# Kernel tuning notes

Measured on AMD Instinct MI355X. Metric: run time of the kernel, lower is better.

## Reference

```python
import jax, jax.numpy as jnp
import numpy as np

B, T, N, K = 1024, 4096, 2048, 16
M = 1 << K  # per-neuron memory size (use_hashing=False -> 2**k)


def setup_inputs() -> dict:
    key = jax.random.key(0)
    k1, k2, k3 = jax.random.split(key, 3)
    input_bits = jax.random.randint(k1, (B, T), 0, 2, dtype=jnp.int32)          # 0/1 bits
    connections = jax.random.randint(k2, (N, K), 0, T, dtype=jnp.int32)         # fixed wiring
    memory = jax.random.randint(k3, (N, M), 0, 256, dtype=jnp.int32)            # per-neuron RAM contents
    return {"input_bits": input_bits, "connections": connections, "memory": memory}


def reference(input_bits, connections, memory):
    # gather the k wired bits for every neuron: [B, N, K]
    gathered = input_bits[:, connections].astype(jnp.int32)
    # bit weights = powers of two (RAMNeuron._bit_weights), LSB-first
    bit_weights = (jnp.int32(1) << jnp.arange(K, dtype=jnp.int32))              # [K]
    # weighted sum -> memory address per (sample, neuron): [B, N]
    addresses = jnp.sum(gathered * bit_weights, axis=-1)
    # per-neuron memory lookup: memory[n, addresses[b, n]] -> [B, N]
    mems = memory[jnp.arange(N)[None, :], addresses]
    # output is the stored LSB as a bool bit
    return (mems & 1).astype(jnp.bool_)
```

## Files before the change

kernel.cpp:

```cpp
#include <hip/hip_runtime.h>
#include <cstdint>

#define Bc 1024
#define Tc 4096
#define Nc 2048
#define Kc 16
#define Mc 65536
#define ROW_WORDS (Mc / 32)
#define PACKED_WORDS ((size_t)Nc * ROW_WORDS)

__global__ __launch_bounds__(256) void pack_kernel(
    const int* __restrict__ memory, uint32_t* __restrict__ packed)
{
    const size_t w = (size_t)blockIdx.x * 256 + threadIdx.x;
    const int4* src = (const int4*)(memory + w * 32);
    uint32_t bw = 0;
#pragma unroll
    for (int i = 0; i < 8; ++i) {
        const int4 v = src[i];
        bw |= (uint32_t)(v.x & 1) << (i * 4);
        bw |= (uint32_t)(v.y & 1) << (i * 4 + 1);
        bw |= (uint32_t)(v.z & 1) << (i * 4 + 2);
        bw |= (uint32_t)(v.w & 1) << (i * 4 + 3);
    }
    packed[w] = bw;
}

__global__ __launch_bounds__(256) void ram_lookup_packed(
    const int* __restrict__ input_bits,
    const int* __restrict__ connections,
    const uint32_t* __restrict__ packedmem,
    int* __restrict__ out)
{
    __shared__ uint32_t bits[Tc / 32];

    const int b    = blockIdx.x;
    const int tid  = threadIdx.x;
    const int lane = tid & 63;
    const int wave = tid >> 6;

    const int* row = input_bits + (size_t)b * Tc;

#pragma unroll
    for (int i = 0; i < Tc / 256; ++i) {
        const int pos = i * 256 + wave * 64 + lane;
        const unsigned long long m = __ballot(row[pos] & 1);
        if (lane == 0) {
            const int w64 = i * 4 + wave;
            bits[w64 * 2]     = (uint32_t)m;
            bits[w64 * 2 + 1] = (uint32_t)(m >> 32);
        }
    }
    __syncthreads();

    uint32_t addrs[Nc / 256];
#pragma unroll
    for (int i = 0; i < Nc / 256; ++i) {
        const int n = i * 256 + tid;
        const int4* cp = (const int4*)(connections + n * Kc);
        const int4 c0 = cp[0], c1 = cp[1], c2 = cp[2], c3 = cp[3];
        const int c[16] = {c0.x, c0.y, c0.z, c0.w,
                           c1.x, c1.y, c1.z, c1.w,
                           c2.x, c2.y, c2.z, c2.w,
                           c3.x, c3.y, c3.z, c3.w};
        uint32_t a = 0;
#pragma unroll
        for (int k = 0; k < 16; ++k) {
            const uint32_t t = (uint32_t)c[k];
            a |= ((bits[t >> 5] >> (t & 31)) & 1u) << k;
        }
        addrs[i] = a;
    }

    uint32_t words[Nc / 256];
#pragma unroll
    for (int i = 0; i < Nc / 256; ++i) {
        const int n = i * 256 + tid;
        words[i] = packedmem[((size_t)n << 11) + (addrs[i] >> 5)];
    }

#pragma unroll
    for (int i = 0; i < Nc / 256; ++i) {
        out[(size_t)b * Nc + i * 256 + tid] = (int)((words[i] >> (addrs[i] & 31)) & 1u);
    }
}

__global__ __launch_bounds__(256) void ram_lookup_direct(
    const int* __restrict__ input_bits,
    const int* __restrict__ connections,
    const int* __restrict__ memory,
    int* __restrict__ out)
{
    __shared__ uint32_t bits[Tc / 32];
    const int b = blockIdx.x, tid = threadIdx.x;
    const int lane = tid & 63, wave = tid >> 6;
    const int* row = input_bits + (size_t)b * Tc;
#pragma unroll
    for (int i = 0; i < Tc / 256; ++i) {
        const int pos = i * 256 + wave * 64 + lane;
        const unsigned long long m = __ballot(row[pos] & 1);
        if (lane == 0) {
            const int w64 = i * 4 + wave;
            bits[w64 * 2] = (uint32_t)m;
            bits[w64 * 2 + 1] = (uint32_t)(m >> 32);
        }
    }
    __syncthreads();
    uint32_t addrs[Nc / 256];
#pragma unroll
    for (int i = 0; i < Nc / 256; ++i) {
        const int n = i * 256 + tid;
        const int4* cp = (const int4*)(connections + n * Kc);
        const int4 c0 = cp[0], c1 = cp[1], c2 = cp[2], c3 = cp[3];
        const int c[16] = {c0.x, c0.y, c0.z, c0.w, c1.x, c1.y, c1.z, c1.w,
                           c2.x, c2.y, c2.z, c2.w, c3.x, c3.y, c3.z, c3.w};
        uint32_t a = 0;
#pragma unroll
        for (int k = 0; k < 16; ++k) {
            const uint32_t t = (uint32_t)c[k];
            a |= ((bits[t >> 5] >> (t & 31)) & 1u) << k;
        }
        addrs[i] = a;
    }
    int vals[Nc / 256];
#pragma unroll
    for (int i = 0; i < Nc / 256; ++i) {
        const int n = i * 256 + tid;
        vals[i] = memory[(size_t)n * Mc + addrs[i]];
    }
#pragma unroll
    for (int i = 0; i < Nc / 256; ++i) {
        out[(size_t)b * Nc + i * 256 + tid] = vals[i] & 1;
    }
}

extern "C" void kernel_launch(void* const* d_in, const int* in_sizes, int n_in,
                              void* d_out, int out_size, void* d_ws, size_t ws_size,
                              hipStream_t stream) {
    const int* input_bits  = (const int*)d_in[0];
    const int* connections = (const int*)d_in[1];
    const int* memory      = (const int*)d_in[2];
    int* out               = (int*)d_out;

    if (ws_size >= PACKED_WORDS * sizeof(uint32_t)) {
        uint32_t* packed = (uint32_t*)d_ws;
        hipLaunchKernelGGL(pack_kernel, dim3(PACKED_WORDS / 256), dim3(256), 0, stream,
                           memory, packed);
        hipLaunchKernelGGL(ram_lookup_packed, dim3(Bc), dim3(256), 0, stream,
                           input_bits, connections, packed, out);
    } else {
        hipLaunchKernelGGL(ram_lookup_direct, dim3(Bc), dim3(256), 0, stream,
                           input_bits, connections, memory, out);
    }
}
```

Before: 727.7 us.

## Replace memory bit-packing with address precompute and neuron-tiled direct gather

The pass that packs the full 512MB memory table into a bit array is removed. Instead, a first kernel computes 16-bit addresses per (sample, neuron) into the workspace, and a second kernel gathers from the original int memory with blocks tiled over neurons, so each block's random reads fall inside a small set of neuron rows. This avoids streaming the whole table every call, at the cost of an address round-trip through global memory and one uncoalesced 4-byte gather per output. The output is written with int4 vector stores.

```diff
diff --git a/kernel.cpp b/kernel.cpp
--- a/kernel.cpp
+++ b/kernel.cpp
@@ -6,31 +6,14 @@
 #define Nc 2048
 #define Kc 16
 #define Mc 65536
-#define ROW_WORDS (Mc / 32)
-#define PACKED_WORDS ((size_t)Nc * ROW_WORDS)
 
-__global__ __launch_bounds__(256) void pack_kernel(
-    const int* __restrict__ memory, uint32_t* __restrict__ packed)
-{
-    const size_t w = (size_t)blockIdx.x * 256 + threadIdx.x;
-    const int4* src = (const int4*)(memory + w * 32);
-    uint32_t bw = 0;
-#pragma unroll
-    for (int i = 0; i < 8; ++i) {
-        const int4 v = src[i];
-        bw |= (uint32_t)(v.x & 1) << (i * 4);
-        bw |= (uint32_t)(v.y & 1) << (i * 4 + 1);
-        bw |= (uint32_t)(v.z & 1) << (i * 4 + 2);
-        bw |= (uint32_t)(v.w & 1) << (i * 4 + 3);
-    }
-    packed[w] = bw;
-}
+#define NTILE 16
+#define ADDR_BYTES ((size_t)Bc * Nc * sizeof(unsigned short))
 
-__global__ __launch_bounds__(256) void ram_lookup_packed(
+__global__ __launch_bounds__(256) void addr_kernel(
     const int* __restrict__ input_bits,
     const int* __restrict__ connections,
-    const uint32_t* __restrict__ packedmem,
-    int* __restrict__ out)
+    unsigned short* __restrict__ addr)
 {
     __shared__ uint32_t bits[Tc / 32];
 
@@ -53,7 +36,6 @@
     }
     __syncthreads();
 
-    uint32_t addrs[Nc / 256];
 #pragma unroll
     for (int i = 0; i < Nc / 256; ++i) {
         const int n = i * 256 + tid;
@@ -69,19 +51,41 @@
             const uint32_t t = (uint32_t)c[k];
             a |= ((bits[t >> 5] >> (t & 31)) & 1u) << k;
         }
-        addrs[i] = a;
+        addr[(size_t)b * Nc + n] = (unsigned short)a;
+    }
+}
+
+__global__ __launch_bounds__(256) void gather_kernel(
+    const unsigned short* __restrict__ addr,
+    const int* __restrict__ memory,
+    int* __restrict__ out)
+{
+    const int n0 = blockIdx.x * NTILE;
+    const int b  = blockIdx.y * 256 + threadIdx.x;
+
+    const uint32_t* ap = (const uint32_t*)(addr + (size_t)b * Nc + n0);
+    uint32_t aw[8];
+#pragma unroll
+    for (int j = 0; j < 8; ++j) aw[j] = ap[j];
+
+    uint32_t a[NTILE];
+#pragma unroll
+    for (int j = 0; j < 8; ++j) {
+        a[2 * j]     = aw[j] & 0xFFFFu;
+        a[2 * j + 1] = aw[j] >> 16;
     }
 
-    uint32_t words[Nc / 256];
+    int v[NTILE];
 #pragma unroll
-    for (int i = 0; i < Nc / 256; ++i) {
-        const int n = i * 256 + tid;
-        words[i] = packedmem[((size_t)n << 11) + (addrs[i] >> 5)];
+    for (int j = 0; j < NTILE; ++j) {
+        v[j] = memory[((size_t)(n0 + j) << 16) + a[j]];
     }
 
+    int4* op = (int4*)(out + (size_t)b * Nc + n0);
 #pragma unroll
-    for (int i = 0; i < Nc / 256; ++i) {
-        out[(size_t)b * Nc + i * 256 + tid] = (int)((words[i] >> (addrs[i] & 31)) & 1u);
+    for (int j = 0; j < 4; ++j) {
+        op[j] = make_int4(v[4 * j] & 1, v[4 * j + 1] & 1,
+                          v[4 * j + 2] & 1, v[4 * j + 3] & 1);
     }
 }
 
@@ -106,7 +110,6 @@
         }
     }
     __syncthreads();
-    uint32_t addrs[Nc / 256];
 #pragma unroll
     for (int i = 0; i < Nc / 256; ++i) {
         const int n = i * 256 + tid;
@@ -120,17 +123,7 @@
             const uint32_t t = (uint32_t)c[k];
             a |= ((bits[t >> 5] >> (t & 31)) & 1u) << k;
         }
-        addrs[i] = a;
-    }
-    int vals[Nc / 256];
-#pragma unroll
-    for (int i = 0; i < Nc / 256; ++i) {
-        const int n = i * 256 + tid;
-        vals[i] = memory[(size_t)n * Mc + addrs[i]];
-    }
-#pragma unroll
-    for (int i = 0; i < Nc / 256; ++i) {
-        out[(size_t)b * Nc + i * 256 + tid] = vals[i] & 1;
+        out[(size_t)b * Nc + n] = memory[(size_t)n * Mc + a] & 1;
     }
 }
 
@@ -142,12 +135,12 @@
     const int* memory      = (const int*)d_in[2];
     int* out               = (int*)d_out;
 
-    if (ws_size >= PACKED_WORDS * sizeof(uint32_t)) {
-        uint32_t* packed = (uint32_t*)d_ws;
-        hipLaunchKernelGGL(pack_kernel, dim3(PACKED_WORDS / 256), dim3(256), 0, stream,
-                           memory, packed);
-        hipLaunchKernelGGL(ram_lookup_packed, dim3(Bc), dim3(256), 0, stream,
-                           input_bits, connections, packed, out);
+    if (ws_size >= ADDR_BYTES) {
+        unsigned short* addr = (unsigned short*)d_ws;
+        hipLaunchKernelGGL(addr_kernel, dim3(Bc), dim3(256), 0, stream,
+                           input_bits, connections, addr);
+        hipLaunchKernelGGL(gather_kernel, dim3(Nc / NTILE, Bc / 256), dim3(256), 0, stream,
+                           addr, memory, out);
     } else {
         hipLaunchKernelGGL(ram_lookup_direct, dim3(Bc), dim3(256), 0, stream,
                            input_bits, connections, memory, out);
```

New measurement: 645.7 us. 11.3% less time.
